# Kernel tuning notes

Measured on AMD Instinct MI355X. Metric: run time of the kernel, lower is better.

## Reference

```python
import jax, jax.numpy as jnp
import numpy as np
import math

B, S, D, H = 8, 512, 512, 8
DH = D // H
MAX_DIST = S - 1
LN_EPS = 1e-5


def _rel_pos_encoding(n_steps, d_model, max_dist):
    # Transformer-XL style sinusoidal table gathered by clipped relative distance
    vocab = 2 * max_dist + 1
    position = np.arange(vocab, dtype=np.float32)[:, None]
    div_term = np.exp(np.arange(0, d_model, 2, dtype=np.float32) * (-math.log(10000.0) / d_model))
    pe = np.zeros((vocab, d_model), dtype=np.float32)
    pe[:, 0::2] = np.sin(position * div_term)
    pe[:, 1::2] = np.cos(position * div_term)
    r = np.arange(n_steps)
    dist = np.clip(r[None, :] - r[:, None], -max_dist, max_dist) + max_dist
    return jnp.asarray(pe[dist])  # [S, S, D]


def setup_inputs() -> dict:
    key = jax.random.key(0)
    ks = jax.random.split(key, 16)
    f32 = jnp.float32
    w = lambda k: jax.random.normal(k, (D, D), dtype=f32) * 0.02
    return {
        "q": jax.random.normal(ks[0], (B, S, D), dtype=f32),
        "k": jax.random.normal(ks[1], (B, S, D), dtype=f32),
        "v": jax.random.normal(ks[2], (B, S, D), dtype=f32),
        "pos_emb": _rel_pos_encoding(S, D, MAX_DIST),
        "Wq": w(ks[3]), "bq": jnp.zeros((D,), f32),
        "Wk": w(ks[4]), "bk": jnp.zeros((D,), f32),
        "Wv": w(ks[5]), "bv": jnp.zeros((D,), f32),
        "Wr": w(ks[6]), "br": jnp.zeros((D,), f32),
        "Wo": w(ks[7]), "bo": jnp.zeros((D,), f32),
        "u_bias": jax.random.normal(ks[8], (H, DH), dtype=f32),
        "v_bias": jax.random.normal(ks[9], (H, DH), dtype=f32),
        "ln_g": jnp.ones((D,), f32),
        "ln_b": jnp.zeros((D,), f32),
    }


def reference(q, k, v, pos_emb, Wq, bq, Wk, bk, Wv, bv, Wr, br, Wo, bo,
              u_bias, v_bias, ln_g, ln_b):
    residual = q
    # projections -> [B, S, H, DH]
    qh = (q @ Wq.T + bq).reshape(B, S, H, DH)
    kh = (k @ Wk.T + bk).reshape(B, S, H, DH)
    vh = (v @ Wv.T + bv).reshape(B, S, H, DH)
    # relative position projection -> [Sq, Sk, H, DH]
    r = (pos_emb @ Wr.T + br).reshape(S, S, H, DH)
    # content-content and content-position scores
    ac = jnp.einsum('bqhd,bkhd->bhqk', qh + u_bias, kh)
    bd = jnp.einsum('bqhd,qkhd->bhqk', qh + v_bias, r)
    attn_score = (ac + bd) / math.sqrt(DH)
    # no key_padding_mask / attn_mask (None in this config) -> plain softmax
    attn_weights = jax.nn.softmax(attn_score, axis=-1)  # [B,H,Sq,Sk]
    attn_out = jnp.einsum('bhqk,bkhd->bqhd', attn_weights, vh).reshape(B, S, D)
    attn_out = attn_out @ Wo.T + bo
    out = residual + attn_out
    # LayerNorm over last dim
    mu = jnp.mean(out, axis=-1, keepdims=True)
    var = jnp.var(out, axis=-1, keepdims=True)
    out = (out - mu) * jax.lax.rsqrt(var + LN_EPS) * ln_g + ln_b
    return out
```

## Files before the change

kernel.cpp:

```cpp
#include <hip/hip_runtime.h>
#include <math.h>

#define B 8
#define S 512
#define D 512
#define H 8
#define DH 64
#define VOCAB (2 * (S - 1) + 1)
#define GK 512

typedef unsigned short u16;
typedef __attribute__((ext_vector_type(8))) short s16x8;
typedef __attribute__((ext_vector_type(4))) float f32x4;

__device__ __forceinline__ u16 f2bf(float f) {
    union { float f; unsigned u; } a; a.f = f;
    unsigned r = a.u + 0x7FFF + ((a.u >> 16) & 1);
    return (u16)(r >> 16);
}
__device__ __forceinline__ float bf2f(u16 h) {
    union { unsigned u; float f; } a; a.u = ((unsigned)h) << 16;
    return a.f;
}
__device__ __forceinline__ void cvt8(const float* __restrict__ s, u16* __restrict__ d) {
    float4 a = *(const float4*)s;
    float4 b = *(const float4*)(s + 4);
    s16x8 o;
    o[0] = f2bf(a.x); o[1] = f2bf(a.y); o[2] = f2bf(a.z); o[3] = f2bf(a.w);
    o[4] = f2bf(b.x); o[5] = f2bf(b.y); o[6] = f2bf(b.z); o[7] = f2bf(b.w);
    *(s16x8*)d = o;
}

#define GLOAD16(gp, lp) __builtin_amdgcn_global_load_lds( \
    (const __attribute__((address_space(1))) unsigned int*)(gp), \
    (__attribute__((address_space(3))) unsigned int*)(lp), 16, 0, 0)

__global__ __launch_bounds__(256) void prep(
    const float* __restrict__ pos_emb,
    const float* __restrict__ q, const float* __restrict__ k, const float* __restrict__ v,
    const float* __restrict__ Wq, const float* __restrict__ Wk, const float* __restrict__ Wv,
    const float* __restrict__ Wr, const float* __restrict__ Wo,
    u16* __restrict__ pe_b, u16* __restrict__ qb, u16* __restrict__ kb, u16* __restrict__ vb,
    u16* __restrict__ Wqb, u16* __restrict__ Wkb, u16* __restrict__ Wvb,
    u16* __restrict__ Wrb, u16* __restrict__ Wob)
{
    const int NPE8 = (1024 * 512) / 8;
    const int NW8  = (512 * 512) / 8;
    const int NBS8 = (B * S * D) / 8;
    const int total = NPE8 + 5 * NW8 + 3 * NBS8;
    for (int i = blockIdx.x * 256 + threadIdx.x; i < total; i += gridDim.x * 256) {
        if (i < NPE8) {
            int e = i * 8;
            int row = e >> 9, col = e & 511;
            if (row >= VOCAB) {
                *(s16x8*)&pe_b[e] = (s16x8)(short)0;
            } else {
                int qq = (row < S) ? (S - 1) : 0;
                int kk = (row < S) ? row : (row - (S - 1));
                cvt8(&pos_emb[(qq * S + kk) * D + col], &pe_b[e]);
            }
            continue;
        }
        int j = i - NPE8;
        if (j < 5 * NW8) {
            int wi = j >> 15;
            int e = (j & (NW8 - 1)) * 8;
            const float* src; u16* dst;
            if      (wi == 0) { src = Wq; dst = Wqb; }
            else if (wi == 1) { src = Wk; dst = Wkb; }
            else if (wi == 2) { src = Wv; dst = Wvb; }
            else if (wi == 3) { src = Wr; dst = Wrb; }
            else              { src = Wo; dst = Wob; }
            cvt8(&src[e], &dst[e]);
            continue;
        }
        int j2 = j - 5 * NW8;
        int qi = j2 >> 18;
        int e = (j2 & (NBS8 - 1)) * 8;
        const float* src; u16* dst;
        if      (qi == 0) { src = q; dst = qb; }
        else if (qi == 1) { src = k; dst = kb; }
        else              { src = v; dst = vb; }
        cvt8(&src[e], &dst[e]);
    }
}

template<bool F32OUT>
__device__ __forceinline__ void gemm128_body(
    const u16* __restrict__ A, const u16* __restrict__ W,
    const float* __restrict__ bias, const float* __restrict__ resid,
    u16* __restrict__ Cb, float* __restrict__ Cf,
    int m0, int n0, u16* As, u16* Ws)
{
    int tid = threadIdx.x;
    int w = tid >> 6, lane = tid & 63;
    int wr = w >> 1, wc = w & 1;
    int lr = lane & 15, lk = lane >> 4;
    f32x4 acc[4][4] = {};

    for (int k0 = 0; k0 < GK; k0 += 64) {
        #pragma unroll
        for (int l = 0; l < 4; ++l) {
            int chunk = w * 4 + l;
            int r = chunk * 8 + (lane >> 3);
            int c = (lane & 7) * 8;
            GLOAD16(&A[(m0 + r) * GK + k0 + c], &As[chunk * 512]);
            GLOAD16(&W[(n0 + r) * GK + k0 + c], &Ws[chunk * 512]);
        }
        __syncthreads();
        #pragma unroll
        for (int ks = 0; ks < 2; ++ks) {
            s16x8 fa[4], fb[4];
            #pragma unroll
            for (int f = 0; f < 4; ++f) {
                fa[f] = *(const s16x8*)&As[(wr * 64 + f * 16 + lr) * 64 + ks * 32 + lk * 8];
                fb[f] = *(const s16x8*)&Ws[(wc * 64 + f * 16 + lr) * 64 + ks * 32 + lk * 8];
            }
            #pragma unroll
            for (int fm = 0; fm < 4; ++fm)
                #pragma unroll
                for (int fn = 0; fn < 4; ++fn)
                    acc[fm][fn] = __builtin_amdgcn_mfma_f32_16x16x32_bf16(
                        fa[fm], fb[fn], acc[fm][fn], 0, 0, 0);
        }
        __syncthreads();
    }
    #pragma unroll
    for (int fm = 0; fm < 4; ++fm) {
        #pragma unroll
        for (int r = 0; r < 4; ++r) {
            int m = m0 + wr * 64 + fm * 16 + lk * 4 + r;
            #pragma unroll
            for (int fn = 0; fn < 4; ++fn) {
                int n = n0 + wc * 64 + fn * 16 + lr;
                float vv = acc[fm][fn][r] + bias[n];
                if (F32OUT) Cf[m * 512 + n] = vv + resid[m * 512 + n];
                else        Cb[m * 512 + n] = f2bf(vv);
            }
        }
    }
}

__global__ __launch_bounds__(256) void proj_qkvr(
    const u16* __restrict__ qb, const u16* __restrict__ kb, const u16* __restrict__ vb,
    const u16* __restrict__ pe_b,
    const u16* __restrict__ Wqb, const u16* __restrict__ Wkb, const u16* __restrict__ Wvb,
    const u16* __restrict__ Wrb,
    const float* __restrict__ bq, const float* __restrict__ bk, const float* __restrict__ bv,
    const float* __restrict__ br,
    u16* __restrict__ qhb, u16* __restrict__ khb, u16* __restrict__ vhb,
    u16* __restrict__ rproj)
{
    __shared__ u16 As[128 * 64];
    __shared__ u16 Ws[128 * 64];
    const u16 *A, *W; const float* bias; u16* C;
    int z = blockIdx.z;
    if      (z == 0) { A = qb;   W = Wqb; bias = bq; C = qhb; }
    else if (z == 1) { A = kb;   W = Wkb; bias = bk; C = khb; }
    else if (z == 2) { A = vb;   W = Wvb; bias = bv; C = vhb; }
    else             { A = pe_b; W = Wrb; bias = br; C = rproj;
                       if (blockIdx.y >= 8) return; }
    gemm128_body<false>(A, W, bias, nullptr, C, nullptr,
                        blockIdx.y * 128, blockIdx.x * 128, As, Ws);
}

__global__ __launch_bounds__(256) void proj_out(
    const u16* __restrict__ aob, const u16* __restrict__ Wob,
    const float* __restrict__ bo, const float* __restrict__ resid,
    float* __restrict__ out)
{
    __shared__ u16 As[128 * 64];
    __shared__ u16 Ws[128 * 64];
    gemm128_body<true>(aob, Wob, bo, resid, nullptr, out,
                       blockIdx.y * 128, blockIdx.x * 128, As, Ws);
}

__global__ __launch_bounds__(256) void attn_mfma(
    const u16* __restrict__ qh, const u16* __restrict__ kh,
    const u16* __restrict__ vh, const u16* __restrict__ rproj,
    const float* __restrict__ u_bias, const float* __restrict__ v_bias,
    u16* __restrict__ ao)
{
    __shared__ u16 K_s[64][72];
    __shared__ u16 Vt_s[64][72];
    __shared__ u16 R_s[128][72];
    __shared__ float T_s[4][16][84];
    __shared__ u16 P_s[4][16][72];

    int bh = blockIdx.x;
    int b = bh >> 3, h = bh & 7;
    int q0 = blockIdx.y * 64;
    int tid = threadIdx.x, w = tid >> 6, lane = tid & 63;
    int lr = lane & 15, lk = lane >> 4;
    int woff = 48 - 16 * w;

    s16x8 qu[2], qv[2];
    {
        int qrow = q0 + 16 * w + lr;
        const u16* qp = &qh[((b * S + qrow) * H + h) * DH];
        #pragma unroll
        for (int f = 0; f < 2; ++f) {
            int d0 = lk * 8 + f * 32;
            s16x8 qraw = *(const s16x8*)&qp[d0];
            s16x8 xu, xv;
            #pragma unroll
            for (int j = 0; j < 8; ++j) {
                float qf = bf2f((u16)qraw[j]);
                xu[j] = (short)f2bf(qf + u_bias[h * DH + d0 + j]);
                xv[j] = (short)f2bf(qf + v_bias[h * DH + d0 + j]);
            }
            qu[f] = xu; qv[f] = xv;
        }
    }

    float m_run[4], l_run[4];
    f32x4 opv[4] = {};
    #pragma unroll
    for (int r = 0; r < 4; ++r) { m_run[r] = -1e30f; l_run[r] = 0.f; }

    for (int kt = 0; kt < 8; ++kt) {
        int k0 = kt * 64;
        int rbase = k0 - q0 + 448;

        #pragma unroll
        for (int i = 0; i < 2; ++i) {
            int g = tid + 256 * i;
            int r = g >> 3, c8 = (g & 7) * 8;
            *(s16x8*)&K_s[r][c8] =
                *(const s16x8*)&kh[((b * S + k0 + r) * H + h) * DH + c8];
        }
        {
            int kk2 = (tid & 31) * 2;
            int n8  = (tid >> 5) * 8;
            const u16* vp = &vh[((b * S + k0 + kk2) * H + h) * DH + n8];
            s16x8 v0 = *(const s16x8*)vp;
            s16x8 v1 = *(const s16x8*)(vp + H * DH);
            #pragma unroll
            for (int e = 0; e < 8; ++e) {
                ushort2 pr; pr.x = (u16)v0[e]; pr.y = (u16)v1[e];
                *(ushort2*)&Vt_s[n8 + e][kk2] = pr;
            }
        }
        #pragma unroll
        for (int i = 0; i < 4; ++i) {
            int g = tid + 256 * i;
            int jr = g >> 3, c8 = (g & 7) * 8;
            int rr = rbase + jr; if (rr > 1022) rr = 1022;
            *(s16x8*)&R_s[jr][c8] =
                *(const s16x8*)&rproj[rr * D + h * DH + c8];
        }
        __syncthreads();

        f32x4 sacc[4] = {};
        #pragma unroll
        for (int ks = 0; ks < 2; ++ks) {
            s16x8 bfr[4];
            #pragma unroll
            for (int cf = 0; cf < 4; ++cf)
                bfr[cf] = *(const s16x8*)&K_s[cf * 16 + lr][ks * 32 + lk * 8];
            #pragma unroll
            for (int cf = 0; cf < 4; ++cf)
                sacc[cf] = __builtin_amdgcn_mfma_f32_16x16x32_bf16(
                    qu[ks], bfr[cf], sacc[cf], 0, 0, 0);
        }
        f32x4 tacc[5] = {};
        #pragma unroll
        for (int ks = 0; ks < 2; ++ks) {
            #pragma unroll
            for (int cf = 0; cf < 5; ++cf) {
                s16x8 bfr = *(const s16x8*)&R_s[woff + cf * 16 + lr][ks * 32 + lk * 8];
                tacc[cf] = __builtin_amdgcn_mfma_f32_16x16x32_bf16(
                    qv[ks], bfr, tacc[cf], 0, 0, 0);
            }
        }
        #pragma unroll
        for (int cf = 0; cf < 5; ++cf)
            #pragma unroll
            for (int r = 0; r < 4; ++r)
                T_s[w][lk * 4 + r][cf * 16 + lr] = tacc[cf][r];
        asm volatile("s_waitcnt lgkmcnt(0)" ::: "memory");

        float sc_f[4][4];
        #pragma unroll
        for (int cf = 0; cf < 4; ++cf)
            #pragma unroll
            for (int r = 0; r < 4; ++r) {
                int ql = lk * 4 + r, kk = lr + cf * 16;
                sc_f[cf][r] = (sacc[cf][r] + T_s[w][ql][kk - ql + 15]) * 0.125f;
            }
        float mt[4];
        #pragma unroll
        for (int r = 0; r < 4; ++r)
            mt[r] = fmaxf(fmaxf(sc_f[0][r], sc_f[1][r]), fmaxf(sc_f[2][r], sc_f[3][r]));
        #pragma unroll
        for (int mask = 1; mask < 16; mask <<= 1)
            #pragma unroll
            for (int r = 0; r < 4; ++r)
                mt[r] = fmaxf(mt[r], __shfl_xor(mt[r], mask, 64));
        float al[4], psum[4];
        #pragma unroll
        for (int r = 0; r < 4; ++r) {
            float mn = fmaxf(m_run[r], mt[r]);
            al[r] = __expf(m_run[r] - mn);
            m_run[r] = mn;
            psum[r] = 0.f;
        }
        #pragma unroll
        for (int cf = 0; cf < 4; ++cf)
            #pragma unroll
            for (int r = 0; r < 4; ++r) {
                float p = __expf(sc_f[cf][r] - m_run[r]);
                psum[r] += p;
                P_s[w][lk * 4 + r][lr + cf * 16] = f2bf(p);
            }
        #pragma unroll
        for (int mask = 1; mask < 16; mask <<= 1)
            #pragma unroll
            for (int r = 0; r < 4; ++r)
                psum[r] += __shfl_xor(psum[r], mask, 64);
        #pragma unroll
        for (int r = 0; r < 4; ++r)
            l_run[r] = l_run[r] * al[r] + psum[r];
        #pragma unroll
        for (int cf = 0; cf < 4; ++cf)
            #pragma unroll
            for (int r = 0; r < 4; ++r)
                opv[cf][r] *= al[r];
        asm volatile("s_waitcnt lgkmcnt(0)" ::: "memory");

        #pragma unroll
        for (int ks = 0; ks < 2; ++ks) {
            s16x8 pa = *(const s16x8*)&P_s[w][lr][ks * 32 + lk * 8];
            #pragma unroll
            for (int cf = 0; cf < 4; ++cf) {
                s16x8 vf = *(const s16x8*)&Vt_s[cf * 16 + lr][ks * 32 + lk * 8];
                opv[cf] = __builtin_amdgcn_mfma_f32_16x16x32_bf16(
                    pa, vf, opv[cf], 0, 0, 0);
            }
        }
        __syncthreads();
    }

    #pragma unroll
    for (int cf = 0; cf < 4; ++cf)
        #pragma unroll
        for (int r = 0; r < 4; ++r) {
            int qrow = q0 + 16 * w + lk * 4 + r;
            ao[((b * S + qrow) * H + h) * DH + lr + 16 * cf] =
                f2bf(opv[cf][r] / l_run[r]);
        }
}

__global__ __launch_bounds__(256) void ln_kernel(
    float* __restrict__ out, const float* __restrict__ g, const float* __restrict__ bta)
{
    int row = blockIdx.x * 4 + threadIdx.x / 64;
    int lane = threadIdx.x % 64;
    float vals[8];
    float sum = 0.f;
    #pragma unroll
    for (int j = 0; j < 8; ++j) {
        vals[j] = out[row * D + lane + j * 64];
        sum += vals[j];
    }
    #pragma unroll
    for (int off = 32; off; off >>= 1) sum += __shfl_xor(sum, off, 64);
    float mu = sum / (float)D;
    float sq = 0.f;
    #pragma unroll
    for (int j = 0; j < 8; ++j) { float dv = vals[j] - mu; sq += dv * dv; }
    #pragma unroll
    for (int off = 32; off; off >>= 1) sq += __shfl_xor(sq, off, 64);
    float rstd = rsqrtf(sq / (float)D + 1e-5f);
    #pragma unroll
    for (int j = 0; j < 8; ++j) {
        int c = lane + j * 64;
        out[row * D + c] = (vals[j] - mu) * rstd * g[c] + bta[c];
    }
}

extern "C" void kernel_launch(void* const* d_in, const int* in_sizes, int n_in,
                              void* d_out, int out_size, void* d_ws, size_t ws_size,
                              hipStream_t stream) {
    const float* q       = (const float*)d_in[0];
    const float* k       = (const float*)d_in[1];
    const float* v       = (const float*)d_in[2];
    const float* pos_emb = (const float*)d_in[3];
    const float* Wq = (const float*)d_in[4];  const float* bq = (const float*)d_in[5];
    const float* Wk = (const float*)d_in[6];  const float* bk = (const float*)d_in[7];
    const float* Wv = (const float*)d_in[8];  const float* bv = (const float*)d_in[9];
    const float* Wr = (const float*)d_in[10]; const float* br = (const float*)d_in[11];
    const float* Wo = (const float*)d_in[12]; const float* bo = (const float*)d_in[13];
    const float* u_bias = (const float*)d_in[14];
    const float* v_bias = (const float*)d_in[15];
    const float* ln_g = (const float*)d_in[16];
    const float* ln_b = (const float*)d_in[17];

    float* out = (float*)d_out;
    u16* ws = (u16*)d_ws;

    const int NBS = B * S * D;
    const int NW  = D * D;
    const int NPE = 1024 * 512;

    u16* pe_b  = ws;
    u16* qb    = pe_b + NPE;
    u16* kb    = qb + NBS;
    u16* vb    = kb + NBS;
    u16* Wqb   = vb + NBS;
    u16* Wkb   = Wqb + NW;
    u16* Wvb   = Wkb + NW;
    u16* Wrb   = Wvb + NW;
    u16* Wob   = Wrb + NW;
    u16* rproj = Wob + NW;
    u16* qhb   = rproj + NPE;
    u16* khb   = qhb + NBS;
    u16* vhb   = khb + NBS;
    u16* aob   = vhb + NBS;

    dim3 blk(256);

    prep<<<2048, blk, 0, stream>>>(pos_emb, q, k, v, Wq, Wk, Wv, Wr, Wo,
                                   pe_b, qb, kb, vb, Wqb, Wkb, Wvb, Wrb, Wob);

    proj_qkvr<<<dim3(4, 32, 4), blk, 0, stream>>>(
        qb, kb, vb, pe_b, Wqb, Wkb, Wvb, Wrb, bq, bk, bv, br,
        qhb, khb, vhb, rproj);

    attn_mfma<<<dim3(B * H, S / 64), blk, 0, stream>>>(qhb, khb, vhb, rproj,
                                                       u_bias, v_bias, aob);

    proj_out<<<dim3(4, 32), blk, 0, stream>>>(aob, Wob, bo, q, out);

    ln_kernel<<<B * S / 4, blk, 0, stream>>>(out, ln_g, ln_b);
}
```

Baseline: 90.48 us.

## Use direct global-to-LDS loads with XOR swizzle and shrink attention LDS footprint

```diff
diff --git a/kernel.cpp b/kernel.cpp
--- a/kernel.cpp
+++ b/kernel.cpp
@@ -175,17 +175,16 @@
                        blockIdx.y * 128, blockIdx.x * 128, As, Ws);
 }
 
-__global__ __launch_bounds__(256) void attn_mfma(
+__global__ __launch_bounds__(256, 2) void attn_mfma(
     const u16* __restrict__ qh, const u16* __restrict__ kh,
     const u16* __restrict__ vh, const u16* __restrict__ rproj,
     const float* __restrict__ u_bias, const float* __restrict__ v_bias,
     u16* __restrict__ ao)
 {
-    __shared__ u16 K_s[64][72];
+    __shared__ u16 K_s[64 * 64];
+    __shared__ u16 R_s[128 * 64];
     __shared__ u16 Vt_s[64][72];
-    __shared__ u16 R_s[128][72];
-    __shared__ float T_s[4][16][84];
-    __shared__ u16 P_s[4][16][72];
+    __shared__ u16 TP_s[4][16][88];
 
     int bh = blockIdx.x;
     int b = bh >> 3, h = bh & 7;
@@ -193,6 +192,8 @@
     int tid = threadIdx.x, w = tid >> 6, lane = tid & 63;
     int lr = lane & 15, lk = lane >> 4;
     int woff = 48 - 16 * w;
+    int swz = (lr & 7) * 8;
+    int c16 = ((lane & 7) ^ (lane >> 3)) * 8;
 
     s16x8 qu[2], qv[2];
     {
@@ -223,11 +224,17 @@
         int rbase = k0 - q0 + 448;
 
         #pragma unroll
-        for (int i = 0; i < 2; ++i) {
-            int g = tid + 256 * i;
-            int r = g >> 3, c8 = (g & 7) * 8;
-            *(s16x8*)&K_s[r][c8] =
-                *(const s16x8*)&kh[((b * S + k0 + r) * H + h) * DH + c8];
+        for (int l = 0; l < 2; ++l) {
+            int chunk = w * 2 + l;
+            int r = chunk * 8 + (lane >> 3);
+            GLOAD16(&kh[((b * S + k0 + r) * H + h) * DH + c16], &K_s[chunk * 512]);
+        }
+        #pragma unroll
+        for (int l = 0; l < 4; ++l) {
+            int chunk = w * 4 + l;
+            int jr = chunk * 8 + (lane >> 3);
+            int rr = rbase + jr; if (rr > 1022) rr = 1022;
+            GLOAD16(&rproj[rr * D + h * DH + c16], &R_s[chunk * 512]);
         }
         {
             int kk2 = (tid & 31) * 2;
@@ -241,14 +248,6 @@
                 *(ushort2*)&Vt_s[n8 + e][kk2] = pr;
             }
         }
-        #pragma unroll
-        for (int i = 0; i < 4; ++i) {
-            int g = tid + 256 * i;
-            int jr = g >> 3, c8 = (g & 7) * 8;
-            int rr = rbase + jr; if (rr > 1022) rr = 1022;
-            *(s16x8*)&R_s[jr][c8] =
-                *(const s16x8*)&rproj[rr * D + h * DH + c8];
-        }
         __syncthreads();
 
         f32x4 sacc[4] = {};
@@ -257,7 +256,7 @@
             s16x8 bfr[4];
             #pragma unroll
             for (int cf = 0; cf < 4; ++cf)
-                bfr[cf] = *(const s16x8*)&K_s[cf * 16 + lr][ks * 32 + lk * 8];
+                bfr[cf] = *(const s16x8*)&K_s[(cf * 16 + lr) * 64 + ((ks * 32 + lk * 8) ^ swz)];
             #pragma unroll
             for (int cf = 0; cf < 4; ++cf)
                 sacc[cf] = __builtin_amdgcn_mfma_f32_16x16x32_bf16(
@@ -268,7 +267,7 @@
         for (int ks = 0; ks < 2; ++ks) {
             #pragma unroll
             for (int cf = 0; cf < 5; ++cf) {
-                s16x8 bfr = *(const s16x8*)&R_s[woff + cf * 16 + lr][ks * 32 + lk * 8];
+                s16x8 bfr = *(const s16x8*)&R_s[(woff + cf * 16 + lr) * 64 + ((ks * 32 + lk * 8) ^ swz)];
                 tacc[cf] = __builtin_amdgcn_mfma_f32_16x16x32_bf16(
                     qv[ks], bfr, tacc[cf], 0, 0, 0);
             }
@@ -277,7 +276,7 @@
         for (int cf = 0; cf < 5; ++cf)
             #pragma unroll
             for (int r = 0; r < 4; ++r)
-                T_s[w][lk * 4 + r][cf * 16 + lr] = tacc[cf][r];
+                TP_s[w][lk * 4 + r][cf * 16 + lr] = f2bf(tacc[cf][r]);
         asm volatile("s_waitcnt lgkmcnt(0)" ::: "memory");
 
         float sc_f[4][4];
@@ -286,7 +285,7 @@
             #pragma unroll
             for (int r = 0; r < 4; ++r) {
                 int ql = lk * 4 + r, kk = lr + cf * 16;
-                sc_f[cf][r] = (sacc[cf][r] + T_s[w][ql][kk - ql + 15]) * 0.125f;
+                sc_f[cf][r] = (sacc[cf][r] + bf2f(TP_s[w][ql][kk - ql + 15])) * 0.125f;
             }
         float mt[4];
         #pragma unroll
@@ -311,7 +310,7 @@
             for (int r = 0; r < 4; ++r) {
                 float p = __expf(sc_f[cf][r] - m_run[r]);
                 psum[r] += p;
-                P_s[w][lk * 4 + r][lr + cf * 16] = f2bf(p);
+                TP_s[w][lk * 4 + r][lr + cf * 16] = f2bf(p);
             }
         #pragma unroll
         for (int mask = 1; mask < 16; mask <<= 1)
@@ -330,7 +329,7 @@
 
         #pragma unroll
         for (int ks = 0; ks < 2; ++ks) {
-            s16x8 pa = *(const s16x8*)&P_s[w][lr][ks * 32 + lk * 8];
+            s16x8 pa = *(const s16x8*)&TP_s[w][lr][ks * 32 + lk * 8];
             #pragma unroll
             for (int cf = 0; cf < 4; ++cf) {
                 s16x8 vf = *(const s16x8*)&Vt_s[cf * 16 + lr][ks * 32 + lk * 8];
```

Result: no change. 89.97 us (-0.6%).
